# Performance work log

Measured on AMD Instinct MI355X. Metric: run time of the kernel, lower is better.

The kernel has to match this reference:

```python
import jax, jax.numpy as jnp
import numpy as np

B, E, R, A, NV, SEL = 512, 1024, 1024, 512, 196, 36

def _lstm_cell(x, h, c, Wih, bih, Whh, bhh):
    g = x @ Wih.T + bih + h @ Whh.T + bhh
    i, f, gg, o = jnp.split(g, 4, axis=1)  # torch gate order i,f,g,o
    c2 = jax.nn.sigmoid(f) * c + jax.nn.sigmoid(i) * jnp.tanh(gg)
    h2 = jax.nn.sigmoid(o) * jnp.tanh(c2)
    return h2, c2

def _attention(h, feats, p_feats, Wh, bh, Wa, ba):
    # feats: [B,S,R], p_feats: [B,S,A]
    att_h = h @ Wh.T + bh                       # [B,A]
    dot = jnp.tanh(p_feats + att_h[:, None, :])  # [B,S,A]
    scores = jnp.einsum('bsa,a->bs', dot, Wa[0]) + ba[0]
    w = jax.nn.softmax(scores, axis=1)
    return jnp.einsum('bs,bsd->bd', w, feats)

def setup_inputs() -> dict:
    key = jax.random.key(0)
    ks = jax.random.split(key, 32)
    s = 0.02
    inp = {
        'xt': jax.random.normal(ks[0], (B, E), jnp.float32),
        'fc_feats': jax.random.normal(ks[1], (B, R), jnp.float32),
        'att_feats': jax.random.normal(ks[2], (B, NV, R), jnp.float32),
        'p_att_feats': jax.random.normal(ks[3], (B, NV, A), jnp.float32),
        'state_h': jax.random.normal(ks[4], (2, B, R), jnp.float32),
        'state_c': jax.random.normal(ks[5], (2, B, R), jnp.float32),
        # att_lstm: input E + 2R
        'W_ih_att': jax.random.normal(ks[6], (4 * R, E + 2 * R), jnp.float32) * s,
        'b_ih_att': jnp.zeros((4 * R,), jnp.float32),
        'W_hh_att': jax.random.normal(ks[7], (4 * R, R), jnp.float32) * s,
        'b_hh_att': jnp.zeros((4 * R,), jnp.float32),
        # lang_lstm: input 3R
        'W_ih_lang': jax.random.normal(ks[8], (4 * R, 3 * R), jnp.float32) * s,
        'b_ih_lang': jnp.zeros((4 * R,), jnp.float32),
        'W_hh_lang': jax.random.normal(ks[9], (4 * R, R), jnp.float32) * s,
        'b_hh_lang': jnp.zeros((4 * R,), jnp.float32),
        # attention 1
        'Wh2att1': jax.random.normal(ks[10], (A, R), jnp.float32) * s,
        'bh2att1': jnp.zeros((A,), jnp.float32),
        'Walpha1': jax.random.normal(ks[11], (1, A), jnp.float32) * s,
        'balpha1': jnp.zeros((1,), jnp.float32),
        # vf attention
        'Wh2att2': jax.random.normal(ks[12], (A, R), jnp.float32) * s,
        'bh2att2': jnp.zeros((A,), jnp.float32),
        'Walpha2': jax.random.normal(ks[13], (1, A), jnp.float32) * s,
        'balpha2': jnp.zeros((1,), jnp.float32),
        # vf_layer and p_vf
        'W_vf': jax.random.normal(ks[14], (NV, 2 * R), jnp.float32) * s,
        'b_vf': jnp.zeros((NV,), jnp.float32),
        'W_pvf': jax.random.normal(ks[15], (A, R), jnp.float32) * s,
        'b_pvf': jnp.zeros((A,), jnp.float32),
    }
    return inp

def reference(xt, fc_feats, att_feats, p_att_feats, state_h, state_c,
              W_ih_att, b_ih_att, W_hh_att, b_hh_att,
              W_ih_lang, b_ih_lang, W_hh_lang, b_hh_lang,
              Wh2att1, bh2att1, Walpha1, balpha1,
              Wh2att2, bh2att2, Walpha2, balpha2,
              W_vf, b_vf, W_pvf, b_pvf):
    # dropout in eval mode -> identity
    prev_h = state_h[-1]
    att_lstm_input = jnp.concatenate([prev_h, fc_feats, xt], axis=1)
    h_att, c_att = _lstm_cell(att_lstm_input, state_h[0], state_c[0],
                              W_ih_att, b_ih_att, W_hh_att, b_hh_att)
    att = _attention(h_att, att_feats, p_att_feats, Wh2att1, bh2att1, Walpha1, balpha1)
    conc = jnp.concatenate([att, h_att], axis=1)          # [B,2R]
    vf_ha = conc @ W_vf.T + b_vf                          # [B,NV]
    vf_soft = jax.nn.softmax(vf_ha, axis=1)
    _, vf_ix = jax.lax.top_k(vf_soft, SEL)                # [B,SEL] (descending)
    arr1 = jnp.take_along_axis(att_feats, vf_ix[:, :, None], axis=1)  # [B,SEL,R]
    p_vf_feats = arr1 @ W_pvf.T + b_pvf                   # [B,SEL,A]
    vf_att = _attention(h_att, arr1, p_vf_feats, Wh2att2, bh2att2, Walpha2, balpha2)
    lang_lstm_input = jnp.concatenate([vf_att, h_att, att], axis=1)
    h_lang, c_lang = _lstm_cell(lang_lstm_input, state_h[1], state_c[1],
                                W_ih_lang, b_ih_lang, W_hh_lang, b_hh_lang)
    output = h_lang
    new_h = jnp.stack([h_att, h_lang])
    new_c = jnp.stack([c_att, c_lang])
    return output, new_h, new_c
```

## Files before the change

kernel.cpp:

```cpp
#include <hip/hip_runtime.h>

typedef __attribute__((ext_vector_type(4))) float f32x4;
typedef __attribute__((ext_vector_type(8))) _Float16 half8;
typedef __attribute__((ext_vector_type(4))) _Float16 half4;

__device__ __forceinline__ float fast_tanh(float x) {
  float e = __expf(2.f * x);
  return 1.f - 2.f / (e + 1.f);
}
__device__ __forceinline__ float fast_sigmoid(float x) {
  return 1.f / (1.f + __expf(-x));
}

__device__ __forceinline__ void gl_lds16(const _Float16* g, _Float16* l) {
  __builtin_amdgcn_global_load_lds(
      (const __attribute__((address_space(1))) void*)g,
      (__attribute__((address_space(3))) void*)l, 16, 0, 0);
}

template<int SPLIT, int OUT16, int NGUARD, int SWAPXY>
__global__ __launch_bounds__(256, SPLIT == 3 ? 2 : 4) void gemm16(
    const _Float16* __restrict__ Ahp, const _Float16* __restrict__ Alp, int lda,
    const _Float16* __restrict__ Bhp, const _Float16* __restrict__ Blp, int ldb,
    void* __restrict__ Cp, int ldc, long czstride,
    int N, int Kc)
{
  __shared__ _Float16 sAh[2][128 * 32];
  __shared__ _Float16 sBh[2][128 * 32];
  __shared__ _Float16 sAl[SPLIT == 3 ? 2 : 1][SPLIT == 3 ? 128 * 32 : 8];
  __shared__ _Float16 sBl[SPLIT == 3 ? 2 : 1][SPLIT == 3 ? 128 * 32 : 8];

  const int tid = threadIdx.x, lane = tid & 63, wid = tid >> 6;
  const int wm = wid >> 1, wn = wid & 1;
  const int l16 = lane & 15, k8 = lane >> 4;
  const int sr = lane >> 2;
  const int scol = ((lane & 3) ^ ((lane >> 3) & 3)) * 8;
  const int koff = ((k8 ^ ((lane >> 1) & 3))) * 8;

  const int  kt0   = blockIdx.z * Kc;
  const long abase = (long)(SWAPXY ? blockIdx.x : blockIdx.y) * 128;
  const long bbase = (long)(SWAPXY ? blockIdx.y : blockIdx.x) * 128;

  const int r0 = wid * 32 + sr;
  const int r1 = wid * 32 + 16 + sr;
  long br0 = bbase + r0, br1 = bbase + r1;
  if (NGUARD) {
    if (br0 > N - 1) br0 = N - 1;
    if (br1 > N - 1) br1 = N - 1;
  }

  const _Float16* ga0 = Ahp + (abase + r0) * (long)lda + kt0 + scol;
  const _Float16* ga1 = Ahp + (abase + r1) * (long)lda + kt0 + scol;
  const _Float16* gb0 = Bhp + br0 * (long)ldb + kt0 + scol;
  const _Float16* gb1 = Bhp + br1 * (long)ldb + kt0 + scol;
  const _Float16* la0 = SPLIT == 3 ? Alp + (abase + r0) * (long)lda + kt0 + scol : nullptr;
  const _Float16* la1 = SPLIT == 3 ? Alp + (abase + r1) * (long)lda + kt0 + scol : nullptr;
  const _Float16* lb0 = SPLIT == 3 ? Blp + br0 * (long)ldb + kt0 + scol : nullptr;
  const _Float16* lb1 = SPLIT == 3 ? Blp + br1 * (long)ldb + kt0 + scol : nullptr;

  const int e0 = (wid * 32) * 32;
  const int e1 = (wid * 32 + 16) * 32;

  f32x4 acc[4][4];
#pragma unroll
  for (int i = 0; i < 4; i++)
#pragma unroll
    for (int j = 0; j < 4; j++) acc[i][j] = (f32x4){0.f, 0.f, 0.f, 0.f};

  auto STAGE = [&](int buf, int kk) {
    gl_lds16(ga0 + kk, &sAh[buf][e0]);
    gl_lds16(ga1 + kk, &sAh[buf][e1]);
    gl_lds16(gb0 + kk, &sBh[buf][e0]);
    gl_lds16(gb1 + kk, &sBh[buf][e1]);
    if (SPLIT == 3) {
      gl_lds16(la0 + kk, &sAl[buf][e0]);
      gl_lds16(la1 + kk, &sAl[buf][e1]);
      gl_lds16(lb0 + kk, &sBl[buf][e0]);
      gl_lds16(lb1 + kk, &sBl[buf][e1]);
    }
  };

  STAGE(0, 0);

  const int nst = Kc >> 5;
  for (int t = 0; t < nst; t++) {
    const int buf = t & 1;
    if (t + 1 < nst) {
      STAGE(buf ^ 1, (t + 1) * 32);
      if (SPLIT == 3) asm volatile("s_waitcnt vmcnt(8)" ::: "memory");
      else            asm volatile("s_waitcnt vmcnt(4)" ::: "memory");
    } else {
      asm volatile("s_waitcnt vmcnt(0)" ::: "memory");
    }
    __builtin_amdgcn_sched_barrier(0);
    __builtin_amdgcn_s_barrier();
    __builtin_amdgcn_sched_barrier(0);

    half8 ah[4], bh[4];
#pragma unroll
    for (int m = 0; m < 4; m++)
      ah[m] = *(const half8*)&sAh[buf][(wm * 64 + m * 16 + l16) * 32 + koff];
#pragma unroll
    for (int n = 0; n < 4; n++)
      bh[n] = *(const half8*)&sBh[buf][(wn * 64 + n * 16 + l16) * 32 + koff];
#pragma unroll
    for (int m = 0; m < 4; m++)
#pragma unroll
      for (int n = 0; n < 4; n++)
        acc[m][n] = __builtin_amdgcn_mfma_f32_16x16x32_f16(ah[m], bh[n], acc[m][n], 0, 0, 0);
    if (SPLIT == 3) {
      half8 al[4], bl[4];
#pragma unroll
      for (int m = 0; m < 4; m++)
        al[m] = *(const half8*)&sAl[buf][(wm * 64 + m * 16 + l16) * 32 + koff];
#pragma unroll
      for (int n = 0; n < 4; n++)
        bl[n] = *(const half8*)&sBl[buf][(wn * 64 + n * 16 + l16) * 32 + koff];
#pragma unroll
      for (int m = 0; m < 4; m++)
#pragma unroll
        for (int n = 0; n < 4; n++) {
          acc[m][n] = __builtin_amdgcn_mfma_f32_16x16x32_f16(al[m], bh[n], acc[m][n], 0, 0, 0);
          acc[m][n] = __builtin_amdgcn_mfma_f32_16x16x32_f16(ah[m], bl[n], acc[m][n], 0, 0, 0);
        }
    }
    __builtin_amdgcn_sched_barrier(0);
    __builtin_amdgcn_s_barrier();
    __builtin_amdgcn_sched_barrier(0);
  }

  const long czoff = (long)blockIdx.z * czstride;
#pragma unroll
  for (int m = 0; m < 4; m++)
#pragma unroll
    for (int n = 0; n < 4; n++) {
      const long row0 = abase + wm * 64 + m * 16 + (lane >> 4) * 4;
      const long col  = bbase + wn * 64 + n * 16 + l16;
      if (!NGUARD || col < N) {
#pragma unroll
        for (int j = 0; j < 4; j++) {
          const long idx = (row0 + j) * (long)ldc + col + czoff;
          if (OUT16) ((_Float16*)Cp)[idx] = (_Float16)acc[m][n][j];
          else       ((float*)Cp)[idx] = acc[m][n][j];
        }
      }
    }
}

__global__ __launch_bounds__(256) void prep_kernel(
    const float* __restrict__ WihA, const float* __restrict__ WhhA,
    const float* __restrict__ WihL, const float* __restrict__ WhhL,
    const float* __restrict__ Wh1, const float* __restrict__ Wh2,
    const float* __restrict__ Wvf, const float* __restrict__ Wpvf,
    const float* __restrict__ xt, const float* __restrict__ fc,
    const float* __restrict__ sh,
    _Float16* __restrict__ WcAh, _Float16* __restrict__ WcAl,
    _Float16* __restrict__ WcLh, _Float16* __restrict__ W12h,
    _Float16* __restrict__ Wvfh, _Float16* __restrict__ Wvfl,
    _Float16* __restrict__ Wpvfh,
    _Float16* __restrict__ X1h, _Float16* __restrict__ X1l)
{
  int bi = blockIdx.x, t = threadIdx.x;
  if (bi < 16384) {
    long e = ((long)bi * 256 + t) * 4;
    int row = (int)(e >> 12), col = (int)(e & 4095);
    const float* src = (col < 3072) ? WihA + (long)row * 3072 + col
                                    : WhhA + (long)row * 1024 + (col - 3072);
    f32x4 v = *(const f32x4*)src;
    half4 h, l;
#pragma unroll
    for (int j = 0; j < 4; j++) { h[j] = (_Float16)v[j]; l[j] = (_Float16)(v[j] - (float)h[j]); }
    *(half4*)&WcAh[e] = h;
    *(half4*)&WcAl[e] = l;
  } else if (bi < 32768) {
    long e = ((long)(bi - 16384) * 256 + t) * 4;
    int row = (int)(e >> 12), col = (int)(e & 4095);
    const float* src = (col < 3072) ? WihL + (long)row * 3072 + col
                                    : WhhL + (long)row * 1024 + (col - 3072);
    f32x4 v = *(const f32x4*)src;
    half4 h;
#pragma unroll
    for (int j = 0; j < 4; j++) h[j] = (_Float16)v[j];
    *(half4*)&WcLh[e] = h;
  } else if (bi < 33792) {
    long e = ((long)(bi - 32768) * 256 + t) * 4;
    int row = (int)(e >> 10), col = (int)(e & 1023);
    const float* src = (row < 512) ? Wh1 + (long)row * 1024 + col
                                   : Wh2 + (long)(row - 512) * 1024 + col;
    f32x4 v = *(const f32x4*)src;
    half4 h;
#pragma unroll
    for (int j = 0; j < 4; j++) h[j] = (_Float16)v[j];
    *(half4*)&W12h[e] = h;
  } else if (bi < 34184) {
    long e = ((long)(bi - 33792) * 256 + t) * 4;
    f32x4 v = *(const f32x4*)(Wvf + e);
    half4 h, l;
#pragma unroll
    for (int j = 0; j < 4; j++) { h[j] = (_Float16)v[j]; l[j] = (_Float16)(v[j] - (float)h[j]); }
    *(half4*)&Wvfh[e] = h;
    *(half4*)&Wvfl[e] = l;
  } else if (bi < 34696) {
    long e = ((long)(bi - 34184) * 256 + t) * 4;
    f32x4 v = *(const f32x4*)(Wpvf + e);
    half4 h;
#pragma unroll
    for (int j = 0; j < 4; j++) h[j] = (_Float16)v[j];
    *(half4*)&Wpvfh[e] = h;
  } else {
    int i = (bi - 34696) * 256 + t;
    int b = i >> 10, rr = i & 1023;
    long base = (long)b * 4096;
    float v[4];
    v[0] = sh[524288 + i];
    v[1] = fc[i];
    v[2] = xt[i];
    v[3] = sh[i];
#pragma unroll
    for (int j = 0; j < 4; j++) {
      _Float16 h = (_Float16)v[j];
      X1h[base + j * 1024 + rr] = h;
      X1l[base + j * 1024 + rr] = (_Float16)(v[j] - (float)h);
    }
  }
}

template<int NP, bool H16, bool ATT>
__global__ __launch_bounds__(256) void lstm_act_kernel(
    const void* __restrict__ gp, const float* __restrict__ bih,
    const float* __restrict__ bhh, const float* __restrict__ cin,
    float* __restrict__ hOut, float* __restrict__ cOut,
    _Float16* __restrict__ hatt_h, _Float16* __restrict__ conch,
    _Float16* __restrict__ concl, _Float16* __restrict__ x2h,
    const float* __restrict__ sh, float* __restrict__ hOut2)
{
  const long S = 2097152;
  int i = blockIdx.x * 256 + threadIdx.x;
  int b = i >> 10, rr = i & 1023;
  long gb = (long)b * 4096;
  float g4[4];
#pragma unroll
  for (int q = 0; q < 4; q++) {
    float s = 0.f;
#pragma unroll
    for (int z = 0; z < NP; z++) {
      long off = (long)z * S + gb + q * 1024 + rr;
      s += H16 ? (float)((const _Float16*)gp)[off] : ((const float*)gp)[off];
    }
    g4[q] = s + bih[q * 1024 + rr] + bhh[q * 1024 + rr];
  }
  float c  = cin[i];
  float c2 = fast_sigmoid(g4[1]) * c + fast_sigmoid(g4[0]) * fast_tanh(g4[2]);
  float h2 = fast_sigmoid(g4[3]) * fast_tanh(c2);
  hOut[i] = h2;
  cOut[i] = c2;
  if (hOut2) hOut2[i] = h2;
  if (ATT) {
    _Float16 hh = (_Float16)h2;
    hatt_h[i] = hh;
    conch[(long)b * 2048 + 1024 + rr] = hh;
    concl[(long)b * 2048 + 1024 + rr] = (_Float16)(h2 - (float)hh);
    x2h[(long)b * 4096 + 1024 + rr] = hh;
    x2h[(long)b * 4096 + 3072 + rr] = (_Float16)sh[524288 + i];
  }
}

__global__ __launch_bounds__(256) void score1_kernel(
    const float* __restrict__ pf, const float* __restrict__ atthp,
    const float* __restrict__ bh,
    const float* __restrict__ walpha, const float* __restrict__ balpha,
    float* __restrict__ out, int nrows)
{
  int gw = blockIdx.x * 4 + (threadIdx.x >> 6);
  int lane = threadIdx.x & 63;
  if (gw >= nrows) return;
  int b = gw / 196;
  const float* p  = pf + (long)gw * 512 + lane * 8;
  const float* bp = bh + lane * 8;
  const float* wp = walpha + lane * 8;
  f32x4 av[2] = {(f32x4){0.f,0.f,0.f,0.f}, (f32x4){0.f,0.f,0.f,0.f}};
#pragma unroll
  for (int z = 0; z < 4; z++) {
    const float* ap = atthp + (long)z * 524288 + (long)b * 1024 + lane * 8;
    av[0] += *(const f32x4*)(ap);
    av[1] += *(const f32x4*)(ap + 4);
  }
  float acc = 0.f;
#pragma unroll
  for (int u = 0; u < 2; u++) {
    f32x4 pv = *(const f32x4*)(p + u * 4);
    f32x4 bv = *(const f32x4*)(bp + u * 4);
    f32x4 wv = *(const f32x4*)(wp + u * 4);
#pragma unroll
    for (int j = 0; j < 4; j++)
      acc += fast_tanh(pv[j] + av[u][j] + bv[j]) * wv[j];
  }
#pragma unroll
  for (int off = 32; off; off >>= 1) acc += __shfl_xor(acc, off);
  if (lane == 0) out[gw] = acc + balpha[0];
}

__global__ __launch_bounds__(256) void attsum1_kernel(
    const float* __restrict__ scores, const float* __restrict__ feats,
    _Float16* __restrict__ conch, _Float16* __restrict__ concl, _Float16* __restrict__ x2h)
{
  __shared__ float w[256];
  int b = blockIdx.x, t = threadIdx.x;
  float s0 = (t < 196) ? scores[b * 196 + t] : -3.0e38f;
  w[t] = s0;
  __syncthreads();
  float mx = -3.0e38f;
  for (int i = 0; i < 196; i++) mx = fmaxf(mx, w[i]);
  float sum = 0.f;
  for (int i = 0; i < 196; i++) sum += __expf(w[i] - mx);
  float inv = 1.f / sum;
  __syncthreads();
  if (t < 196) w[t] = __expf(s0 - mx) * inv;
  __syncthreads();
  f32x4 acc = (f32x4){0.f, 0.f, 0.f, 0.f};
  const float* fb = feats + (long)b * 200704 + t * 4;
  for (int s0i = 0; s0i < 192; s0i += 8) {
    f32x4 v[8];
#pragma unroll
    for (int u = 0; u < 8; u++) v[u] = *(const f32x4*)(fb + (long)(s0i + u) * 1024);
#pragma unroll
    for (int u = 0; u < 8; u++) {
      float ws = w[s0i + u];
#pragma unroll
      for (int j = 0; j < 4; j++) acc[j] += ws * v[u][j];
    }
  }
#pragma unroll
  for (int u = 192; u < 196; u++) {
    float ws = w[u];
    f32x4 v = *(const f32x4*)(fb + (long)u * 1024);
#pragma unroll
    for (int j = 0; j < 4; j++) acc[j] += ws * v[j];
  }
  half4 h, l;
#pragma unroll
  for (int j = 0; j < 4; j++) { h[j] = (_Float16)acc[j]; l[j] = (_Float16)(acc[j] - (float)h[j]); }
  *(half4*)&conch[(long)b * 2048 + t * 4] = h;
  *(half4*)&concl[(long)b * 2048 + t * 4] = l;
  *(half4*)&x2h[(long)b * 4096 + 2048 + t * 4] = h;
}

__global__ __launch_bounds__(256) void vfatt_kernel(
    const _Float16* __restrict__ pvf16, const float* __restrict__ atthp,
    const float* __restrict__ bh2att2, const float* __restrict__ b_pvf,
    const float* __restrict__ walpha2, const float* __restrict__ balpha2,
    const _Float16* __restrict__ arr1h, _Float16* __restrict__ x2h)
{
  __shared__ float w[40];
  int b = blockIdx.x, tid = threadIdx.x;
  int lane = tid & 63, wv = tid >> 6;

  float add[8], wal[8];
#pragma unroll
  for (int u = 0; u < 8; u++) {
    int a = lane * 8 + u;
    add[u] = bh2att2[a] + b_pvf[a];
    wal[u] = walpha2[a];
  }
#pragma unroll
  for (int z = 0; z < 4; z++) {
    const float* ap = atthp + (long)z * 524288 + (long)b * 1024 + 512 + lane * 8;
#pragma unroll
    for (int u = 0; u < 8; u++) add[u] += ap[u];
  }
  for (int j = wv; j < 36; j += 4) {
    half8 hv = *(const half8*)&pvf16[((long)b * 36 + j) * 512 + lane * 8];
    float acc = 0.f;
#pragma unroll
    for (int u = 0; u < 8; u++)
      acc += fast_tanh((float)hv[u] + add[u]) * wal[u];
#pragma unroll
    for (int off = 32; off; off >>= 1) acc += __shfl_xor(acc, off);
    if (lane == 0) w[j] = acc + balpha2[0];
  }
  __syncthreads();
  float mx = -3.0e38f;
  for (int i = 0; i < 36; i++) mx = fmaxf(mx, w[i]);
  float sum = 0.f;
  for (int i = 0; i < 36; i++) sum += __expf(w[i] - mx);
  float inv = 1.f / sum;
  __syncthreads();
  if (tid < 36) w[tid] = __expf(w[tid] - mx) * inv;
  __syncthreads();
  f32x4 acc = (f32x4){0.f, 0.f, 0.f, 0.f};
  const _Float16* fb = arr1h + (long)b * 36 * 1024 + tid * 4;
#pragma unroll 4
  for (int s = 0; s < 36; s++) {
    float ws = w[s];
    half4 v = *(const half4*)(fb + (long)s * 1024);
#pragma unroll
    for (int j = 0; j < 4; j++) acc[j] += ws * (float)v[j];
  }
  half4 h;
#pragma unroll
  for (int j = 0; j < 4; j++) h[j] = (_Float16)acc[j];
  *(half4*)&x2h[(long)b * 4096 + tid * 4] = h;
}

template<int NP>
__global__ __launch_bounds__(64) void topk_kernel(
    const float* __restrict__ vfp, const float* __restrict__ b_vf, int* __restrict__ ix)
{
  int b = blockIdx.x;
  int lane = threadIdx.x;
  float v[4];
#pragma unroll
  for (int j = 0; j < 4; j++) {
    int s = lane + 64 * j;
    float sum = -3.0e38f;
    if (s < 196) {
      sum = b_vf[s];
#pragma unroll
      for (int z = 0; z < NP; z++) sum += vfp[(long)z * 100352 + b * 196 + s];
    }
    v[j] = sum;
  }
  for (int it = 0; it < 36; it++) {
    float bv = -3.0e38f; int bs = 1 << 20;
#pragma unroll
    for (int j = 0; j < 4; j++) {
      int s = lane + 64 * j;
      if (v[j] > bv) { bv = v[j]; bs = s; }
    }
#pragma unroll
    for (int off = 32; off; off >>= 1) {
      float ov = __shfl_xor(bv, off);
      int   os = __shfl_xor(bs, off);
      if (ov > bv || (ov == bv && os < bs)) { bv = ov; bs = os; }
    }
    if ((bs & 63) == lane) v[bs >> 6] = -3.0e38f;
    if (lane == 0) ix[b * 36 + it] = bs;
  }
}

__global__ __launch_bounds__(256) void gather_conv_kernel(
    const float* __restrict__ feats, const int* __restrict__ ix, _Float16* __restrict__ dst)
{
  int bj = blockIdx.x;
  int b = bj / 36;
  int s = ix[bj];
  int t = threadIdx.x;
  f32x4 v = *(const f32x4*)(feats + ((long)b * 196 + s) * 1024 + t * 4);
  half4 h;
#pragma unroll
  for (int j = 0; j < 4; j++) h[j] = (_Float16)v[j];
  *(half4*)&dst[(long)bj * 1024 + t * 4] = h;
}

extern "C" void kernel_launch(void* const* d_in, const int* in_sizes, int n_in,
                              void* d_out, int out_size, void* d_ws, size_t ws_size,
                              hipStream_t stream) {
  const float* xt        = (const float*)d_in[0];
  const float* fc_feats  = (const float*)d_in[1];
  const float* att_feats = (const float*)d_in[2];
  const float* p_att     = (const float*)d_in[3];
  const float* state_h   = (const float*)d_in[4];
  const float* state_c   = (const float*)d_in[5];
  const float* b_ih_att  = (const float*)d_in[7];
  const float* b_hh_att  = (const float*)d_in[9];
  const float* b_ih_lang = (const float*)d_in[11];
  const float* b_hh_lang = (const float*)d_in[13];
  const float* bh2att1   = (const float*)d_in[15];
  const float* Walpha1   = (const float*)d_in[16];
  const float* balpha1   = (const float*)d_in[17];
  const float* bh2att2   = (const float*)d_in[19];
  const float* Walpha2   = (const float*)d_in[20];
  const float* balpha2   = (const float*)d_in[21];
  const float* b_vf      = (const float*)d_in[23];
  const float* b_pvf     = (const float*)d_in[25];

  float* out = (float*)d_out;
  float* W = (float*)d_ws;

  _Float16* WcAh   = (_Float16*)(W + 0);
  _Float16* WcAl   = (_Float16*)(W + 8388608);
  _Float16* WcLh   = (_Float16*)(W + 16777216);
  _Float16* X1h    = (_Float16*)(W + 25165824);
  _Float16* X1l    = (_Float16*)(W + 26214400);
  float*    g1p    = W + 27262976;
  _Float16* hatt_h = (_Float16*)(W + 35651584);
  _Float16* W12h   = (_Float16*)(W + 35913728);
  _Float16* Wvfh   = (_Float16*)(W + 36438016);
  _Float16* Wvfl   = (_Float16*)(W + 36638720);
  _Float16* Wpvfh  = (_Float16*)(W + 36839424);
  float*    atthp  = W + 37101568;
  _Float16* conch  = (_Float16*)(W + 39198720);
  _Float16* concl  = (_Float16*)(W + 39723008);
  _Float16* X2h    = (_Float16*)(W + 40247296);
  float*    scores1= W + 41295872;
  float*    vfhap  = W + 41396224;
  int*      vfix   = (int*)(W + 43001856);
  _Float16* arr1h  = (_Float16*)(W + 43020288);
  _Float16* pvf16  = (_Float16*)(W + 52457472);
  _Float16* g2ph   = (_Float16*)(W + 57176064);

  float* out_h0 = out + 524288;
  float* out_h1 = out + 2 * 524288;
  float* out_c0 = out + 3 * 524288;
  float* out_c1 = out + 4 * 524288;

  prep_kernel<<<36744, 256, 0, stream>>>(
      (const float*)d_in[6], (const float*)d_in[8],
      (const float*)d_in[10], (const float*)d_in[12],
      (const float*)d_in[14], (const float*)d_in[18],
      (const float*)d_in[22], (const float*)d_in[24],
      xt, fc_feats, state_h,
      WcAh, WcAl, WcLh, W12h, Wvfh, Wvfl, Wpvfh, X1h, X1l);

  gemm16<3, 0, 0, 0><<<dim3(32, 4, 4), 256, 0, stream>>>(
      X1h, X1l, 4096, WcAh, WcAl, 4096, g1p, 4096, 2097152, 4096, 1024);

  lstm_act_kernel<4, false, true><<<2048, 256, 0, stream>>>(
      g1p, b_ih_att, b_hh_att, state_c, out_h0, out_c0,
      hatt_h, conch, concl, X2h, state_h, nullptr);

  gemm16<1, 0, 0, 0><<<dim3(8, 4, 4), 256, 0, stream>>>(
      hatt_h, nullptr, 1024, W12h, nullptr, 1024, atthp, 1024, 524288, 1024, 256);

  score1_kernel<<<25088, 256, 0, stream>>>(
      p_att, atthp, bh2att1, Walpha1, balpha1, scores1, 100352);

  attsum1_kernel<<<512, 256, 0, stream>>>(scores1, att_feats, conch, concl, X2h);

  gemm16<3, 0, 1, 0><<<dim3(2, 4, 16), 256, 0, stream>>>(
      conch, concl, 2048, Wvfh, Wvfl, 2048, vfhap, 196, 100352, 196, 128);

  topk_kernel<16><<<512, 64, 0, stream>>>(vfhap, b_vf, vfix);

  gather_conv_kernel<<<18432, 256, 0, stream>>>(att_feats, vfix, arr1h);

  gemm16<1, 1, 0, 1><<<dim3(144, 4, 1), 256, 0, stream>>>(
      arr1h, nullptr, 1024, Wpvfh, nullptr, 1024, pvf16, 512, 0, 512, 1024);

  vfatt_kernel<<<512, 256, 0, stream>>>(
      pvf16, atthp, bh2att2, b_pvf, Walpha2, balpha2, arr1h, X2h);

  gemm16<1, 1, 0, 0><<<dim3(32, 4, 8), 256, 0, stream>>>(
      X2h, nullptr, 4096, WcLh, nullptr, 4096, g2ph, 4096, 2097152, 4096, 512);

  lstm_act_kernel<8, true, false><<<2048, 256, 0, stream>>>(
      g2ph, b_ih_lang, b_hh_lang, state_c + 524288, out, out_c1,
      nullptr, nullptr, nullptr, nullptr, nullptr, out_h1);
}
```

Baseline: 425.4 us.

## Switch GEMM to 32x32x16 MFMA tiles and halve lang-LSTM split-K

Rewrites the gemm16 inner loop to use 32x32x16 f16 MFMA instructions with 2x2 accumulator tiles per wave instead of 4x4 tiles of 16x16x32, with new LDS swizzled k-offsets and a matching output index mapping. It also drops the min-occupancy hint from launch_bounds and cuts split-K for the language-LSTM GEMM from 8 to 4, doubling Kc. The aim is fewer MFMA issues and LDS fragment loads per k-step, plus less partial-sum traffic for the reduction in lstm_act. The trade-offs are fewer blocks in flight for the lang GEMM and possible register-pressure or occupancy changes.

```diff
diff --git a/kernel.cpp b/kernel.cpp
--- a/kernel.cpp
+++ b/kernel.cpp
@@ -1,6 +1,7 @@
 #include <hip/hip_runtime.h>
 
 typedef __attribute__((ext_vector_type(4))) float f32x4;
+typedef __attribute__((ext_vector_type(16))) float f32x16;
 typedef __attribute__((ext_vector_type(8))) _Float16 half8;
 typedef __attribute__((ext_vector_type(4))) _Float16 half4;
 
@@ -19,7 +20,7 @@
 }
 
 template<int SPLIT, int OUT16, int NGUARD, int SWAPXY>
-__global__ __launch_bounds__(256, SPLIT == 3 ? 2 : 4) void gemm16(
+__global__ __launch_bounds__(256) void gemm16(
     const _Float16* __restrict__ Ahp, const _Float16* __restrict__ Alp, int lda,
     const _Float16* __restrict__ Bhp, const _Float16* __restrict__ Blp, int ldb,
     void* __restrict__ Cp, int ldc, long czstride,
@@ -32,10 +33,13 @@
 
   const int tid = threadIdx.x, lane = tid & 63, wid = tid >> 6;
   const int wm = wid >> 1, wn = wid & 1;
-  const int l16 = lane & 15, k8 = lane >> 4;
+  const int l32 = lane & 31, h32 = lane >> 5;
   const int sr = lane >> 2;
   const int scol = ((lane & 3) ^ ((lane >> 3) & 3)) * 8;
-  const int koff = ((k8 ^ ((lane >> 1) & 3))) * 8;
+  const int rswz = (l32 >> 1) & 3;
+  int ko[2];
+  ko[0] = ((h32)     ^ rswz) * 8;
+  ko[1] = ((2 + h32) ^ rswz) * 8;
 
   const int  kt0   = blockIdx.z * Kc;
   const long abase = (long)(SWAPXY ? blockIdx.x : blockIdx.y) * 128;
@@ -61,11 +65,13 @@
   const int e0 = (wid * 32) * 32;
   const int e1 = (wid * 32 + 16) * 32;
 
-  f32x4 acc[4][4];
-#pragma unroll
-  for (int i = 0; i < 4; i++)
-#pragma unroll
-    for (int j = 0; j < 4; j++) acc[i][j] = (f32x4){0.f, 0.f, 0.f, 0.f};
+  f32x16 acc[2][2];
+#pragma unroll
+  for (int i = 0; i < 2; i++)
+#pragma unroll
+    for (int j = 0; j < 2; j++)
+#pragma unroll
+      for (int r = 0; r < 16; r++) acc[i][j][r] = 0.f;
 
   auto STAGE = [&](int buf, int kk) {
     gl_lds16(ga0 + kk, &sAh[buf][e0]);
@@ -96,33 +102,48 @@
     __builtin_amdgcn_s_barrier();
     __builtin_amdgcn_sched_barrier(0);
 
-    half8 ah[4], bh[4];
-#pragma unroll
-    for (int m = 0; m < 4; m++)
-      ah[m] = *(const half8*)&sAh[buf][(wm * 64 + m * 16 + l16) * 32 + koff];
-#pragma unroll
-    for (int n = 0; n < 4; n++)
-      bh[n] = *(const half8*)&sBh[buf][(wn * 64 + n * 16 + l16) * 32 + koff];
-#pragma unroll
-    for (int m = 0; m < 4; m++)
-#pragma unroll
-      for (int n = 0; n < 4; n++)
-        acc[m][n] = __builtin_amdgcn_mfma_f32_16x16x32_f16(ah[m], bh[n], acc[m][n], 0, 0, 0);
+    half8 a0[2][2], b0[2][2];
+#pragma unroll
+    for (int mt = 0; mt < 2; mt++)
+#pragma unroll
+      for (int ks = 0; ks < 2; ks++)
+        a0[mt][ks] = *(const half8*)&sAh[buf][(wm * 64 + mt * 32 + l32) * 32 + ko[ks]];
+#pragma unroll
+    for (int nt = 0; nt < 2; nt++)
+#pragma unroll
+      for (int ks = 0; ks < 2; ks++)
+        b0[nt][ks] = *(const half8*)&sBh[buf][(wn * 64 + nt * 32 + l32) * 32 + ko[ks]];
+#pragma unroll
+    for (int mt = 0; mt < 2; mt++)
+#pragma unroll
+      for (int nt = 0; nt < 2; nt++)
+#pragma unroll
+        for (int ks = 0; ks < 2; ks++)
+          acc[mt][nt] = __builtin_amdgcn_mfma_f32_32x32x16_f16(
+              a0[mt][ks], b0[nt][ks], acc[mt][nt], 0, 0, 0);
     if (SPLIT == 3) {
-      half8 al[4], bl[4];
-#pragma unroll
-      for (int m = 0; m < 4; m++)
-        al[m] = *(const half8*)&sAl[buf][(wm * 64 + m * 16 + l16) * 32 + koff];
-#pragma unroll
-      for (int n = 0; n < 4; n++)
-        bl[n] = *(const half8*)&sBl[buf][(wn * 64 + n * 16 + l16) * 32 + koff];
-#pragma unroll
-      for (int m = 0; m < 4; m++)
-#pragma unroll
-        for (int n = 0; n < 4; n++) {
-          acc[m][n] = __builtin_amdgcn_mfma_f32_16x16x32_f16(al[m], bh[n], acc[m][n], 0, 0, 0);
-          acc[m][n] = __builtin_amdgcn_mfma_f32_16x16x32_f16(ah[m], bl[n], acc[m][n], 0, 0, 0);
-        }
+      half8 al_[2][2], bl_[2][2];
+#pragma unroll
+      for (int mt = 0; mt < 2; mt++)
+#pragma unroll
+        for (int ks = 0; ks < 2; ks++)
+          al_[mt][ks] = *(const half8*)&sAl[buf][(wm * 64 + mt * 32 + l32) * 32 + ko[ks]];
+#pragma unroll
+      for (int nt = 0; nt < 2; nt++)
+#pragma unroll
+        for (int ks = 0; ks < 2; ks++)
+          bl_[nt][ks] = *(const half8*)&sBl[buf][(wn * 64 + nt * 32 + l32) * 32 + ko[ks]];
+#pragma unroll
+      for (int mt = 0; mt < 2; mt++)
+#pragma unroll
+        for (int nt = 0; nt < 2; nt++)
+#pragma unroll
+          for (int ks = 0; ks < 2; ks++) {
+            acc[mt][nt] = __builtin_amdgcn_mfma_f32_32x32x16_f16(
+                al_[mt][ks], b0[nt][ks], acc[mt][nt], 0, 0, 0);
+            acc[mt][nt] = __builtin_amdgcn_mfma_f32_32x32x16_f16(
+                a0[mt][ks], bl_[nt][ks], acc[mt][nt], 0, 0, 0);
+          }
     }
     __builtin_amdgcn_sched_barrier(0);
     __builtin_amdgcn_s_barrier();
@@ -131,17 +152,18 @@
 
   const long czoff = (long)blockIdx.z * czstride;
 #pragma unroll
-  for (int m = 0; m < 4; m++)
-#pragma unroll
-    for (int n = 0; n < 4; n++) {
-      const long row0 = abase + wm * 64 + m * 16 + (lane >> 4) * 4;
-      const long col  = bbase + wn * 64 + n * 16 + l16;
+  for (int mt = 0; mt < 2; mt++)
+#pragma unroll
+    for (int nt = 0; nt < 2; nt++) {
+      const long rowb = abase + wm * 64 + mt * 32;
+      const long col  = bbase + wn * 64 + nt * 32 + l32;
       if (!NGUARD || col < N) {
 #pragma unroll
-        for (int j = 0; j < 4; j++) {
-          const long idx = (row0 + j) * (long)ldc + col + czoff;
-          if (OUT16) ((_Float16*)Cp)[idx] = (_Float16)acc[m][n][j];
-          else       ((float*)Cp)[idx] = acc[m][n][j];
+        for (int r = 0; r < 16; r++) {
+          const long row = rowb + (r & 3) + 8 * (r >> 2) + 4 * h32;
+          const long idx = row * (long)ldc + col + czoff;
+          if (OUT16) ((_Float16*)Cp)[idx] = (_Float16)acc[mt][nt][r];
+          else       ((float*)Cp)[idx] = acc[mt][nt][r];
         }
       }
     }
@@ -540,10 +562,10 @@
   vfatt_kernel<<<512, 256, 0, stream>>>(
       pvf16, atthp, bh2att2, b_pvf, Walpha2, balpha2, arr1h, X2h);
 
-  gemm16<1, 1, 0, 0><<<dim3(32, 4, 8), 256, 0, stream>>>(
-      X2h, nullptr, 4096, WcLh, nullptr, 4096, g2ph, 4096, 2097152, 4096, 512);
-
-  lstm_act_kernel<8, true, false><<<2048, 256, 0, stream>>>(
+  gemm16<1, 1, 0, 0><<<dim3(32, 4, 4), 256, 0, stream>>>(
+      X2h, nullptr, 4096, WcLh, nullptr, 4096, g2ph, 4096, 2097152, 4096, 1024);
+
+  lstm_act_kernel<4, true, false><<<2048, 256, 0, stream>>>(
       g2ph, b_ih_lang, b_hh_lang, state_c + 524288, out, out_c1,
       nullptr, nullptr, nullptr, nullptr, nullptr, out_h1);
 }
```

New measurement: 428.3 us. No clear change (+0.7%).

## Fuse attention scoring with softmax-sum and top-k with gather, cut split-K

Applied to the files above, without the earlier changes.

Merges the per-row attention score kernel into the softmax/weighted-sum kernel so each batch block computes its 196 scores in shared memory, removing the scores buffer round trip and one launch. Likewise fuses top-k selection with the feature gather and half conversion into one block per batch row. The language LSTM GEMM split-K factor drops from 8 to 4, halving partial-sum traffic for the activation kernel. The occupancy hint on the GEMM launch bounds is also removed. Fewer, larger fused blocks may reduce parallelism for the scoring phase.

```diff
diff --git a/kernel.cpp b/kernel.cpp
--- a/kernel.cpp
+++ b/kernel.cpp
@@ -19,7 +19,7 @@
 }
 
 template<int SPLIT, int OUT16, int NGUARD, int SWAPXY>
-__global__ __launch_bounds__(256, SPLIT == 3 ? 2 : 4) void gemm16(
+__global__ __launch_bounds__(256) void gemm16(
     const _Float16* __restrict__ Ahp, const _Float16* __restrict__ Alp, int lda,
     const _Float16* __restrict__ Bhp, const _Float16* __restrict__ Blp, int ldb,
     void* __restrict__ Cp, int ldc, long czstride,
@@ -265,58 +265,55 @@
   }
 }
 
-__global__ __launch_bounds__(256) void score1_kernel(
+__global__ __launch_bounds__(256) void att1_kernel(
     const float* __restrict__ pf, const float* __restrict__ atthp,
     const float* __restrict__ bh,
     const float* __restrict__ walpha, const float* __restrict__ balpha,
-    float* __restrict__ out, int nrows)
+    const float* __restrict__ feats,
+    _Float16* __restrict__ conch, _Float16* __restrict__ concl,
+    _Float16* __restrict__ x2h)
 {
-  int gw = blockIdx.x * 4 + (threadIdx.x >> 6);
-  int lane = threadIdx.x & 63;
-  if (gw >= nrows) return;
-  int b = gw / 196;
-  const float* p  = pf + (long)gw * 512 + lane * 8;
-  const float* bp = bh + lane * 8;
-  const float* wp = walpha + lane * 8;
-  f32x4 av[2] = {(f32x4){0.f,0.f,0.f,0.f}, (f32x4){0.f,0.f,0.f,0.f}};
+  __shared__ float w[200];
+  int b = blockIdx.x, t = threadIdx.x;
+  int lane = t & 63, wv = t >> 6;
+
+  f32x4 add0 = *(const f32x4*)(bh + lane * 8);
+  f32x4 add1 = *(const f32x4*)(bh + lane * 8 + 4);
 #pragma unroll
   for (int z = 0; z < 4; z++) {
     const float* ap = atthp + (long)z * 524288 + (long)b * 1024 + lane * 8;
-    av[0] += *(const f32x4*)(ap);
-    av[1] += *(const f32x4*)(ap + 4);
-  }
-  float acc = 0.f;
-#pragma unroll
-  for (int u = 0; u < 2; u++) {
-    f32x4 pv = *(const f32x4*)(p + u * 4);
-    f32x4 bv = *(const f32x4*)(bp + u * 4);
-    f32x4 wv = *(const f32x4*)(wp + u * 4);
-#pragma unroll
-    for (int j = 0; j < 4; j++)
-      acc += fast_tanh(pv[j] + av[u][j] + bv[j]) * wv[j];
-  }
-#pragma unroll
-  for (int off = 32; off; off >>= 1) acc += __shfl_xor(acc, off);
-  if (lane == 0) out[gw] = acc + balpha[0];
-}
-
-__global__ __launch_bounds__(256) void attsum1_kernel(
-    const float* __restrict__ scores, const float* __restrict__ feats,
-    _Float16* __restrict__ conch, _Float16* __restrict__ concl, _Float16* __restrict__ x2h)
-{
-  __shared__ float w[256];
-  int b = blockIdx.x, t = threadIdx.x;
-  float s0 = (t < 196) ? scores[b * 196 + t] : -3.0e38f;
-  w[t] = s0;
-  __syncthreads();
+    add0 += *(const f32x4*)(ap);
+    add1 += *(const f32x4*)(ap + 4);
+  }
+  f32x4 wv0 = *(const f32x4*)(walpha + lane * 8);
+  f32x4 wv1 = *(const f32x4*)(walpha + lane * 8 + 4);
+
+  for (int s = wv; s < 196; s += 4) {
+    const float* p = pf + ((long)b * 196 + s) * 512 + lane * 8;
+    f32x4 p0 = *(const f32x4*)(p);
+    f32x4 p1 = *(const f32x4*)(p + 4);
+    float acc = 0.f;
+#pragma unroll
+    for (int j = 0; j < 4; j++) {
+      acc += fast_tanh(p0[j] + add0[j]) * wv0[j];
+      acc += fast_tanh(p1[j] + add1[j]) * wv1[j];
+    }
+#pragma unroll
+    for (int off = 32; off; off >>= 1) acc += __shfl_xor(acc, off);
+    if (lane == 0) w[s] = acc + balpha[0];
+  }
+  __syncthreads();
+
   float mx = -3.0e38f;
   for (int i = 0; i < 196; i++) mx = fmaxf(mx, w[i]);
   float sum = 0.f;
   for (int i = 0; i < 196; i++) sum += __expf(w[i] - mx);
   float inv = 1.f / sum;
-  __syncthreads();
-  if (t < 196) w[t] = __expf(s0 - mx) * inv;
-  __syncthreads();
+  float myw = (t < 196) ? __expf(w[t] - mx) * inv : 0.f;
+  __syncthreads();
+  if (t < 196) w[t] = myw;
+  __syncthreads();
+
   f32x4 acc = (f32x4){0.f, 0.f, 0.f, 0.f};
   const float* fb = feats + (long)b * 200704 + t * 4;
   for (int s0i = 0; s0i < 192; s0i += 8) {
@@ -343,6 +340,59 @@
   *(half4*)&conch[(long)b * 2048 + t * 4] = h;
   *(half4*)&concl[(long)b * 2048 + t * 4] = l;
   *(half4*)&x2h[(long)b * 4096 + 2048 + t * 4] = h;
+}
+
+template<int NP>
+__global__ __launch_bounds__(256) void topk_gather_kernel(
+    const float* __restrict__ vfp, const float* __restrict__ b_vf,
+    const float* __restrict__ feats, _Float16* __restrict__ dst)
+{
+  __shared__ float sv[196];
+  __shared__ int six[36];
+  int b = blockIdx.x, t = threadIdx.x;
+
+  if (t < 196) {
+    float s = b_vf[t];
+#pragma unroll
+    for (int z = 0; z < NP; z++) s += vfp[(long)z * 100352 + b * 196 + t];
+    sv[t] = s;
+  }
+  __syncthreads();
+
+  if (t < 64) {
+    float v[4];
+#pragma unroll
+    for (int j = 0; j < 4; j++) {
+      int s = t + 64 * j;
+      v[j] = (s < 196) ? sv[s] : -3.0e38f;
+    }
+    for (int it = 0; it < 36; it++) {
+      float bv = -3.0e38f; int bs = 1 << 20;
+#pragma unroll
+      for (int j = 0; j < 4; j++) {
+        int s = t + 64 * j;
+        if (v[j] > bv) { bv = v[j]; bs = s; }
+      }
+#pragma unroll
+      for (int off = 32; off; off >>= 1) {
+        float ov = __shfl_xor(bv, off);
+        int   os = __shfl_xor(bs, off);
+        if (ov > bv || (ov == bv && os < bs)) { bv = ov; bs = os; }
+      }
+      if ((bs & 63) == t) v[bs >> 6] = -3.0e38f;
+      if (t == 0) six[it] = bs;
+    }
+  }
+  __syncthreads();
+
+  for (int j = 0; j < 36; j++) {
+    int s = six[j];
+    f32x4 v = *(const f32x4*)(feats + ((long)b * 196 + s) * 1024 + t * 4);
+    half4 h;
+#pragma unroll
+    for (int q = 0; q < 4; q++) h[q] = (_Float16)v[q];
+    *(half4*)&dst[((long)b * 36 + j) * 1024 + t * 4] = h;
+  }
 }
 
 __global__ __launch_bounds__(256) void vfatt_kernel(
@@ -400,56 +450,6 @@
 #pragma unroll
   for (int j = 0; j < 4; j++) h[j] = (_Float16)acc[j];
   *(half4*)&x2h[(long)b * 4096 + tid * 4] = h;
-}
-
-template<int NP>
-__global__ __launch_bounds__(64) void topk_kernel(
-    const float* __restrict__ vfp, const float* __restrict__ b_vf, int* __restrict__ ix)
-{
-  int b = blockIdx.x;
-  int lane = threadIdx.x;
-  float v[4];
-#pragma unroll
-  for (int j = 0; j < 4; j++) {
-    int s = lane + 64 * j;
-    float sum = -3.0e38f;
-    if (s < 196) {
-      sum = b_vf[s];
-#pragma unroll
-      for (int z = 0; z < NP; z++) sum += vfp[(long)z * 100352 + b * 196 + s];
-    }
-    v[j] = sum;
-  }
-  for (int it = 0; it < 36; it++) {
-    float bv = -3.0e38f; int bs = 1 << 20;
-#pragma unroll
-    for (int j = 0; j < 4; j++) {
-      int s = lane + 64 * j;
-      if (v[j] > bv) { bv = v[j]; bs = s; }
-    }
-#pragma unroll
-    for (int off = 32; off; off >>= 1) {
-      float ov = __shfl_xor(bv, off);
-      int   os = __shfl_xor(bs, off);
-      if (ov > bv || (ov == bv && os < bs)) { bv = ov; bs = os; }
-    }
-    if ((bs & 63) == lane) v[bs >> 6] = -3.0e38f;
-    if (lane == 0) ix[b * 36 + it] = bs;
-  }
-}
-
-__global__ __launch_bounds__(256) void gather_conv_kernel(
-    const float* __restrict__ feats, const int* __restrict__ ix, _Float16* __restrict__ dst)
-{
-  int bj = blockIdx.x;
-  int b = bj / 36;
-  int s = ix[bj];
-  int t = threadIdx.x;
-  f32x4 v = *(const f32x4*)(feats + ((long)b * 196 + s) * 1024 + t * 4);
-  half4 h;
-#pragma unroll
-  for (int j = 0; j < 4; j++) h[j] = (_Float16)v[j];
-  *(half4*)&dst[(long)bj * 1024 + t * 4] = h;
 }
 
 extern "C" void kernel_launch(void* const* d_in, const int* in_sizes, int n_in,
@@ -492,9 +492,7 @@
   _Float16* conch  = (_Float16*)(W + 39198720);
   _Float16* concl  = (_Float16*)(W + 39723008);
   _Float16* X2h    = (_Float16*)(W + 40247296);
-  float*    scores1= W + 41295872;
   float*    vfhap  = W + 41396224;
-  int*      vfix   = (int*)(W + 43001856);
   _Float16* arr1h  = (_Float16*)(W + 43020288);
   _Float16* pvf16  = (_Float16*)(W + 52457472);
   _Float16* g2ph   = (_Float16*)(W + 57176064);
@@ -522,17 +520,13 @@
   gemm16<1, 0, 0, 0><<<dim3(8, 4, 4), 256, 0, stream>>>(
       hatt_h, nullptr, 1024, W12h, nullptr, 1024, atthp, 1024, 524288, 1024, 256);
 
-  score1_kernel<<<25088, 256, 0, stream>>>(
-      p_att, atthp, bh2att1, Walpha1, balpha1, scores1, 100352);
-
-  attsum1_kernel<<<512, 256, 0, stream>>>(scores1, att_feats, conch, concl, X2h);
+  att1_kernel<<<512, 256, 0, stream>>>(
+      p_att, atthp, bh2att1, Walpha1, balpha1, att_feats, conch, concl, X2h);
 
   gemm16<3, 0, 1, 0><<<dim3(2, 4, 16), 256, 0, stream>>>(
       conch, concl, 2048, Wvfh, Wvfl, 2048, vfhap, 196, 100352, 196, 128);
 
-  topk_kernel<16><<<512, 64, 0, stream>>>(vfhap, b_vf, vfix);
-
-  gather_conv_kernel<<<18432, 256, 0, stream>>>(att_feats, vfix, arr1h);
+  topk_gather_kernel<16><<<512, 256, 0, stream>>>(vfhap, b_vf, att_feats, arr1h);
 
   gemm16<1, 1, 0, 1><<<dim3(144, 4, 1), 256, 0, stream>>>(
       arr1h, nullptr, 1024, Wpvfh, nullptr, 1024, pvf16, 512, 0, 512, 1024);
@@ -540,10 +534,10 @@
   vfatt_kernel<<<512, 256, 0, stream>>>(
       pvf16, atthp, bh2att2, b_pvf, Walpha2, balpha2, arr1h, X2h);
 
-  gemm16<1, 1, 0, 0><<<dim3(32, 4, 8), 256, 0, stream>>>(
-      X2h, nullptr, 4096, WcLh, nullptr, 4096, g2ph, 4096, 2097152, 4096, 512);
-
-  lstm_act_kernel<8, true, false><<<2048, 256, 0, stream>>>(
+  gemm16<1, 1, 0, 0><<<dim3(32, 4, 4), 256, 0, stream>>>(
+      X2h, nullptr, 4096, WcLh, nullptr, 4096, g2ph, 4096, 2097152, 4096, 1024);
+
+  lstm_act_kernel<4, true, false><<<2048, 256, 0, stream>>>(
       g2ph, b_ih_lang, b_hh_lang, state_c + 524288, out, out_c1,
       nullptr, nullptr, nullptr, nullptr, nullptr, out_h1);
 }
```

Result: faster. 414.1 us (-2.7%).
